# Kernel optimization log

Measured on AMD Instinct MI355X. Metric: run time of the kernel, lower is better.

Reference implementation:

```python
import jax, jax.numpy as jnp
import numpy as np

B, C, N, T = 8, 64, 170, 512
LEAK = 0.01
TEMP = 0.5


def _conv2d(x, w, b):
    # x: [B,C,N,Tp], w: [O,I,1,k] -> valid conv along time
    y = jax.lax.conv_general_dilated(x, w, (1, 1), 'VALID',
                                     dimension_numbers=('NCHW', 'OIHW', 'NCHW'))
    return y + b[None, :, None, None]


def _branch(x, w5, b5, w3, b3):
    # ReplicationPad2d((3,3,0,0)) -> Conv(1,5) -> LeakyReLU -> Conv(1,3) -> Tanh
    xp = jnp.pad(x, ((0, 0), (0, 0), (0, 0), (3, 3)), mode='edge')
    h = _conv2d(xp, w5, b5)
    h = jnp.where(h >= 0, h, LEAK * h)
    h = _conv2d(h, w3, b3)
    return jnp.tanh(h)


def _diff_gcn(x, adj, w, b):
    # Diffusion_GCN, support_len=1, order=1: concat([x, x@adj]) -> 1x1 conv
    x1 = jnp.einsum('bcnt,nm->bcmt', x, adj)
    h = jnp.concatenate([x, x1], axis=1)  # [B,2C,N,T]
    return jnp.einsum('bknt,ok->bont', h, w[:, :, 0, 0]) + b[None, :, None, None]


def _gumbel(k, shape, eps=1e-20):
    u = jax.random.uniform(k, shape, jnp.float32)
    return -jnp.log(-jnp.log(u + eps) + eps)


def _graph_gen(x, adj, g, ggw, ggb, fc0w, fc0b, fc1w, fc1b, fc2w, fc2b):
    h = _diff_gcn(x, adj, ggw, ggb)          # [B,C,N,T]
    h = h[-1].sum(-1).T                      # last batch elem, sum over T -> [N,C]
    h = jnp.tanh(h @ fc0w.T + fc0b)
    h = jnp.tanh(h @ fc1w.T + fc1b)
    h = jnp.tanh(h @ fc2w.T + fc2b)
    logp = jax.nn.log_softmax(h, axis=-1)
    y_soft = jax.nn.softmax((logp + g) / TEMP, axis=-1)
    y_hard = jax.nn.one_hot(jnp.argmax(y_soft, axis=-1), y_soft.shape[-1], dtype=y_soft.dtype)
    y = jax.lax.stop_gradient(y_hard - y_soft) + y_soft  # straight-through
    return y * (1.0 - jnp.eye(y.shape[0], dtype=y.dtype))  # zero diagonal


def _forward(x, nv1, nv2, a, c1w5, c1b5, c1w3, c1b3, c2w5, c2b5, c2w3, c2b3,
             c3w5, c3b5, c3w3, c3b3, c4w5, c4b5, c4w3, c4b3,
             ggw, ggb, fc0w, fc0b, fc1w, fc1b, fc2w, fc2b, dcw, dcb, gs):
    adj = jax.nn.softmax(jax.nn.relu(nv1 @ nv2), axis=1)
    xe, xo = x[..., ::2], x[..., 1::2]
    gg = (ggw, ggb, fc0w, fc0b, fc1w, fc1b, fc2w, fc2b)

    def step(xin, w5, b5, w3, b3, g):
        h = _branch(xin, w5, b5, w3, b3)
        la = _graph_gen(h, adj, g, *gg)
        dadj = la * a + adj * (1.0 - a)
        return h + _diff_gcn(h, dadj, dcw, dcb), dadj

    x1, dadj = step(xe, c1w5, c1b5, c1w3, c1b3, gs[0])
    d = xo * jnp.tanh(x1)
    x2, dadj = step(xo, c2w5, c2b5, c2w3, c2b3, gs[1])
    c = xe * jnp.tanh(x2)
    x3, dadj = step(c, c3w5, c3b5, c3w3, c3b3, gs[2])
    x_odd_update = d - x3
    x4, dadj = step(d, c4w5, c4b5, c4w3, c4b3, gs[3])
    x_even_update = c + x4
    return x_even_update, x_odd_update, dadj


def setup_inputs() -> dict:
    key = jax.random.key(0)
    ks = jax.random.split(key, 16)

    def rn(i, shape, s):
        return jax.random.normal(ks[i], shape, jnp.float32) * s

    inp = {'x': rn(0, (B, C, N, T), 1.0),
           'nv1': rn(1, (N, 10), 1.0),
           'nv2': rn(2, (10, N), 1.0),
           'a': jnp.array([0.5], jnp.float32)}
    i = 3
    for p in ('c1', 'c2', 'c3', 'c4'):
        inp[p + 'w5'] = rn(i, (C, C, 1, 5), 0.05); i += 1
        inp[p + 'b5'] = jnp.zeros((C,), jnp.float32)
        inp[p + 'w3'] = rn(i, (C, C, 1, 3), 0.05); i += 1
        inp[p + 'b3'] = jnp.zeros((C,), jnp.float32)
    inp['ggw'] = rn(i, (C, 2 * C, 1, 1), 0.08); i += 1
    inp['ggb'] = jnp.zeros((C,), jnp.float32)
    inp['fc0w'] = rn(i, (N, C), 0.1); i += 1
    inp['fc0b'] = jnp.zeros((N,), jnp.float32)
    inp['fc1w'] = rn(i, (2 * N, N), 0.06); i += 1
    inp['fc1b'] = jnp.zeros((2 * N,), jnp.float32)
    inp['fc2w'] = rn(i, (N, 2 * N), 0.05); i += 1
    inp['fc2b'] = jnp.zeros((N,), jnp.float32)
    inp['dcw'] = rn(i, (C, 2 * C, 1, 1), 0.08); i += 1
    inp['dcb'] = jnp.zeros((C,), jnp.float32)
    return inp


def reference(x, nv1, nv2, a, c1w5, c1b5, c1w3, c1b3, c2w5, c2b5, c2w3, c2b3,
              c3w5, c3b5, c3w3, c3b3, c4w5, c4b5, c4w3, c4b3,
              ggw, ggb, fc0w, fc0b, fc1w, fc1b, fc2w, fc2b, dcw, dcb):
    n = nv1.shape[0]
    gk = jax.random.split(jax.random.key(42), 4)
    gs = tuple(_gumbel(k, (n, n)) for k in gk)
    return _forward(x, nv1, nv2, a, c1w5, c1b5, c1w3, c1b3, c2w5, c2b5, c2w3, c2b3,
                    c3w5, c3b5, c3w3, c3b3, c4w5, c4b5, c4w3, c4b3,
                    ggw, ggb, fc0w, fc0b, fc1w, fc1b, fc2w, fc2b, dcw, dcb, gs)
```

## Files before the change

### kernel.cpp

```cpp
#include <hip/hip_runtime.h>
#include <hip/hip_bf16.h>
#include <cstdint>
#include <cstddef>

using bf16 = __hip_bfloat16;

static constexpr int BBATCH = 8, CCH = 64, NNODE = 170, TT = 256;
static constexpr size_t HSZ  = (size_t)BBATCH * CCH * NNODE * TT;
static constexpr size_t H7SZ = (size_t)CCH * NNODE * TT;
static constexpr int GN = NNODE * NNODE;

typedef __attribute__((ext_vector_type(8))) short short8v;
typedef __attribute__((ext_vector_type(4))) float f32x4;

__device__ __forceinline__ float b2f(bf16 v) { return __bfloat162float(v); }
__device__ __forceinline__ bf16  f2b(float v) { return __float2bfloat16(v); }

union BfU { bf16 h; unsigned short s; };
__device__ __forceinline__ unsigned short bfbits(float v) { BfU u; u.h = f2b(v); return u.s; }
__device__ __forceinline__ unsigned pack2(float a, float b) {
  return ((unsigned)bfbits(b) << 16) | bfbits(a);
}
__device__ __forceinline__ unsigned pks(short lo, short hi) {
  return ((unsigned)(unsigned short)hi << 16) | (unsigned short)lo;
}
__device__ __forceinline__ float shortbf(short s) { BfU u; u.s = (unsigned short)s; return b2f(u.h); }

__device__ __forceinline__ float tanhfast(float v) {
  float e = __expf(2.f * v);
  return 1.f - 2.f / (e + 1.f);
}

__device__ __forceinline__ unsigned rotl32(unsigned v, int d) { return (v << d) | (v >> (32 - d)); }

__device__ void threefry2x32(unsigned k0, unsigned k1, unsigned x0, unsigned x1,
                             unsigned& y0, unsigned& y1) {
  unsigned ks0 = k0, ks1 = k1, ks2 = k0 ^ k1 ^ 0x1BD11BDAu;
  x0 += ks0; x1 += ks1;
  const int ra[4] = {13, 15, 26, 6};
  const int rb[4] = {17, 29, 16, 24};
#pragma unroll
  for (int r = 0; r < 4; r++) { x0 += x1; x1 = rotl32(x1, ra[r]); x1 ^= x0; }
  x0 += ks1; x1 += ks2 + 1u;
#pragma unroll
  for (int r = 0; r < 4; r++) { x0 += x1; x1 = rotl32(x1, rb[r]); x1 ^= x0; }
  x0 += ks2; x1 += ks0 + 2u;
#pragma unroll
  for (int r = 0; r < 4; r++) { x0 += x1; x1 = rotl32(x1, ra[r]); x1 ^= x0; }
  x0 += ks0; x1 += ks1 + 3u;
#pragma unroll
  for (int r = 0; r < 4; r++) { x0 += x1; x1 = rotl32(x1, rb[r]); x1 ^= x0; }
  x0 += ks1; x1 += ks2 + 4u;
#pragma unroll
  for (int r = 0; r < 4; r++) { x0 += x1; x1 = rotl32(x1, ra[r]); x1 ^= x0; }
  x0 += ks2; x1 += ks0 + 5u;
  y0 = x0; y1 = x1;
}

struct SetupArgs {
  const float* w5[4]; const float* w3[4];
  float* wT5[4]; float* wT3[4];
  short* wp5[4]; short* wp3[4];
  const float* dcw; short* dcwP;
  const float* nv1; const float* nv2; float* adj;
  float* g;
};

__global__ __launch_bounds__(256) void k_setup(SetupArgs a) {
  const int blk = blockIdx.x;
  const int tid = threadIdx.x;
  __shared__ float red[256];

  if (blk < 170) {
    const int i = blk, j = tid;
    float val = 0.f, r = -1e30f;
    if (j < NNODE) {
      float acc = 0.f;
      for (int k = 0; k < 10; k++) acc += a.nv1[i*10+k] * a.nv2[k*NNODE+j];
      val = acc > 0.f ? acc : 0.f;
      r = val;
    }
    red[j] = r; __syncthreads();
    for (int s = 128; s; s >>= 1) { if (j < s) red[j] = fmaxf(red[j], red[j+s]); __syncthreads(); }
    float m = red[0]; __syncthreads();
    float e = (j < NNODE) ? expf(val - m) : 0.f;
    red[j] = e; __syncthreads();
    for (int s = 128; s; s >>= 1) { if (j < s) red[j] += red[j+s]; __syncthreads(); }
    if (j < NNODE) a.adj[i*NNODE+j] = e / red[0];
    return;
  }
  if (blk < 622) {
    int idx = (blk - 170) * 256 + tid;
    if (idx >= 4 * GN) return;
    int w = idx / GN, i = idx % GN;
    unsigned k0, k1, y0, y1;
    threefry2x32(0u, 42u, 0u, (unsigned)w, k0, k1);
    threefry2x32(k0, k1, 0u, (unsigned)i, y0, y1);
    unsigned bits = y0 ^ y1;
    unsigned fb = (bits >> 9) | 0x3f800000u;
    float u = __uint_as_float(fb) - 1.0f;
    a.g[idx] = -logf(-logf(u + 1e-20f) + 1e-20f);
    return;
  }
  if (blk < 942) {
    int gi = blk - 622, s = gi / 80;
    int idx = (gi - s*80) * 256 + tid;
    if (idx >= 20480) return;
    int oc = idx / 5, k = idx - oc * 5;
    int o = oc >> 6, c = oc & 63;
    a.wT5[s][(c*5 + k)*64 + o] = a.w5[s][idx];
    return;
  }
  if (blk < 1134) {
    int gi = blk - 942, s = gi / 48;
    int idx = (gi - s*48) * 256 + tid;
    if (idx >= 12288) return;
    int oc = idx / 3, k = idx - oc * 3;
    int o = oc >> 6, c = oc & 63;
    a.wT3[s][(c*3 + k)*64 + o] = a.w3[s][idx];
    return;
  }
  if (blk < 1454) {
    int gi = blk - 1134, s = gi / 80;
    int idx = (gi - s*80) * 256 + tid;
    if (idx >= 20480) return;
    int j = idx & 7, l = (idx >> 3) & 63, mi = (idx >> 9) & 3, ks = (idx >> 11) & 1, k = idx >> 12;
    int o = mi*16 + (l & 15);
    int c = ks*32 + (l >> 4)*8 + j;
    a.wp5[s][idx] = (short)bfbits(a.w5[s][(o*64 + c)*5 + k]);
    return;
  }
  if (blk < 1646) {
    int gi = blk - 1454, s = gi / 48;
    int idx = (gi - s*48) * 256 + tid;
    if (idx >= 12288) return;
    int j = idx & 7, l = (idx >> 3) & 63, mi = (idx >> 9) & 3, ks = (idx >> 11) & 1, k = idx >> 12;
    int o = mi*16 + (l & 15);
    int c = ks*32 + (l >> 4)*8 + j;
    a.wp3[s][idx] = (short)bfbits(a.w3[s][(o*64 + c)*3 + k]);
    return;
  }
  {
    int idx = (blk - 1646) * 256 + tid;
    if (idx >= 8192) return;
    int j = idx & 7, l = (idx >> 3) & 63, mi = (idx >> 9) & 3, kk = idx >> 11;
    int o = mi*16 + (l & 15);
    int c = kk*32 + (l >> 4)*8 + j;
    a.dcwP[idx] = (short)bfbits(a.dcw[o*128 + c]);
  }
}

__device__ void branch_body(int n, int q, int b,
    const float* __restrict__ src, int par,
    const float* __restrict__ wT5, const float* __restrict__ b5,
    const float* __restrict__ wT3, const float* __restrict__ b3,
    const short* __restrict__ wp5, const short* __restrict__ wp3,
    bf16* __restrict__ hout, float* __restrict__ h7f, float* __restrict__ Spart,
    char* lds) {
  const int tid = threadIdx.x;
  const int l = tid & 63;
  const int w = __builtin_amdgcn_readfirstlane(tid >> 6);
  const int t0 = q * 64;

  if (b == 7) {
    float (*xs)[72]  = (float(*)[72])lds;
    float (*h1s)[68] = (float(*)[68])(lds + 18432);
    const int o = l;
    const int base = w * 16;
    const bool w3x = (w == 3);

    for (int i = tid; i < 64 * 70; i += 256) {
      int c = i / 70, pl = i - c * 70;
      int t = t0 + pl - 3; t = t < 0 ? 0 : (t > 255 ? 255 : t);
      size_t sb = ((size_t)7 * 64 + c) * NNODE + n;
      xs[c][pl] = (par >= 0) ? src[sb * 512 + 2 * t + par] : src[sb * 256 + t];
    }
    __syncthreads();

    {
      float acc[16];
#pragma unroll
      for (int tt = 0; tt < 16; tt++) acc[tt] = 0.f;
      float aH0 = 0.f, aH1 = 0.f;
      const float* wp = wT5 + o;
      for (int c = 0; c < 64; c++) {
        float xv[22];
        float4 v0 = *(const float4*)&xs[c][base + 0];
        float4 v1 = *(const float4*)&xs[c][base + 4];
        float4 v2 = *(const float4*)&xs[c][base + 8];
        float4 v3 = *(const float4*)&xs[c][base + 12];
        float4 v4 = *(const float4*)&xs[c][base + 16];
        xv[0]=v0.x; xv[1]=v0.y; xv[2]=v0.z; xv[3]=v0.w;
        xv[4]=v1.x; xv[5]=v1.y; xv[6]=v1.z; xv[7]=v1.w;
        xv[8]=v2.x; xv[9]=v2.y; xv[10]=v2.z; xv[11]=v2.w;
        xv[12]=v3.x; xv[13]=v3.y; xv[14]=v3.z; xv[15]=v3.w;
        xv[16]=v4.x; xv[17]=v4.y; xv[18]=v4.z; xv[19]=v4.w;
        if (w3x) { float2 vt = *(const float2*)&xs[c][68]; xv[20]=vt.x; xv[21]=vt.y; }
        float w0 = wp[0], w1 = wp[64], w2 = wp[128], w3_ = wp[192], w4 = wp[256];
        wp += 320;
#pragma unroll
        for (int tt = 0; tt < 16; tt++)
          acc[tt] += w0*xv[tt] + w1*xv[tt+1] + w2*xv[tt+2] + w3_*xv[tt+3] + w4*xv[tt+4];
        if (w3x) {
          aH0 += w0*xv[16] + w1*xv[17] + w2*xv[18] + w3_*xv[19] + w4*xv[20];
          aH1 += w0*xv[17] + w1*xv[18] + w2*xv[19] + w3_*xv[20] + w4*xv[21];
        }
      }
      float bias = b5[o];
#pragma unroll
      for (int tt = 0; tt < 16; tt++) {
        float v = acc[tt] + bias;
        h1s[o][base + tt] = v >= 0.f ? v : 0.01f * v;
      }
      if (w3x) {
        float u0 = aH0 + bias, u1 = aH1 + bias;
        h1s[o][64] = u0 >= 0.f ? u0 : 0.01f * u0;
        h1s[o][65] = u1 >= 0.f ? u1 : 0.01f * u1;
      }
    }
    __syncthreads();

    {
      float acc[16];
#pragma unroll
      for (int tt = 0; tt < 16; tt++) acc[tt] = 0.f;
      const float* wp = wT3 + o;
      for (int c = 0; c < 64; c++) {
        float hv[18];
        float4 v0 = *(const float4*)&h1s[c][base + 0];
        float4 v1 = *(const float4*)&h1s[c][base + 4];
        float4 v2 = *(const float4*)&h1s[c][base + 8];
        float4 v3 = *(const float4*)&h1s[c][base + 12];
        float4 v4 = *(const float4*)&h1s[c][base + 16];
        hv[0]=v0.x; hv[1]=v0.y; hv[2]=v0.z; hv[3]=v0.w;
        hv[4]=v1.x; hv[5]=v1.y; hv[6]=v1.z; hv[7]=v1.w;
        hv[8]=v2.x; hv[9]=v2.y; hv[10]=v2.z; hv[11]=v2.w;
        hv[12]=v3.x; hv[13]=v3.y; hv[14]=v3.z; hv[15]=v3.w;
        hv[16]=v4.x; hv[17]=v4.y;
        float w0 = wp[0], w1 = wp[64], w2 = wp[128];
        wp += 192;
#pragma unroll
        for (int tt = 0; tt < 16; tt++)
          acc[tt] += w0*hv[tt] + w1*hv[tt+1] + w2*hv[tt+2];
      }
      float bias = b3[o];
#pragma unroll
      for (int tt = 0; tt < 16; tt++) acc[tt] = tanhf(acc[tt] + bias);
      __syncthreads();
#pragma unroll
      for (int tt = 0; tt < 16; tt++) xs[o][base + tt] = acc[tt];
    }
    __syncthreads();

    {
      const int ro = tid >> 2, rq = tid & 3;
      float4 v0 = *(const float4*)&xs[ro][rq*16 + 0];
      float4 v1 = *(const float4*)&xs[ro][rq*16 + 4];
      float4 v2 = *(const float4*)&xs[ro][rq*16 + 8];
      float4 v3 = *(const float4*)&xs[ro][rq*16 + 12];
      float* dst = h7f + ((size_t)ro * NNODE + n) * TT + t0 + rq*16;
      *(float4*)&dst[0] = v0; *(float4*)&dst[4] = v1;
      *(float4*)&dst[8] = v2; *(float4*)&dst[12] = v3;
      float s = v0.x+v0.y+v0.z+v0.w + v1.x+v1.y+v1.z+v1.w
              + v2.x+v2.y+v2.z+v2.w + v3.x+v3.y+v3.z+v3.w;
      s += __shfl_xor(s, 1, 4);
      s += __shfl_xor(s, 2, 4);
      if (rq == 0) Spart[(q * 64 + ro) * NNODE + n] = s;
    }
    return;
  }

  const int mi = w;

  {
    int t = t0 + l - 3; t = t < 0 ? 0 : (t > 255 ? 255 : t);
#pragma unroll
    for (int it = 0; it < 8; it++) {
      int c0 = it * 8 + mi * 2;
      size_t sb = ((size_t)b * 64 + c0) * NNODE + n;
      float v0, v1;
      if (par >= 0) { v0 = src[sb * 512 + 2*t + par]; v1 = src[(sb + NNODE) * 512 + 2*t + par]; }
      else          { v0 = src[sb * 256 + t];         v1 = src[(sb + NNODE) * 256 + t]; }
      *(unsigned*)(lds + l*128 + ((2*c0) ^ ((l & 7) << 4))) = pack2(v0, v1);
    }
  }
  if (tid < 192) {
    int tr = 64 + (tid >> 5);
    int c0 = (tid & 31) * 2;
    int t = t0 + tr - 3; if (t > 255) t = 255;
    size_t sb = ((size_t)b * 64 + c0) * NNODE + n;
    float v0, v1;
    if (par >= 0) { v0 = src[sb * 512 + 2*t + par]; v1 = src[(sb + NNODE) * 512 + 2*t + par]; }
    else          { v0 = src[sb * 256 + t];         v1 = src[(sb + NNODE) * 256 + t]; }
    *(unsigned*)(lds + tr*128 + ((2*c0) ^ ((tr & 7) << 4))) = pack2(v0, v1);
  }
  __syncthreads();

  f32x4 acc[5];
#pragma unroll
  for (int i = 0; i < 5; i++) acc[i] = (f32x4){0.f, 0.f, 0.f, 0.f};
  for (int k = 0; k < 5; k++) {
#pragma unroll
    for (int ks = 0; ks < 2; ks++) {
      short8v af = *(const short8v*)(wp5 + (size_t)((((k*2 + ks)*4 + mi)*64 + l) * 8));
      const int c0 = ks*32 + (l >> 4)*8;
#pragma unroll
      for (int ni = 0; ni < 5; ni++) {
        int tr = ni*16 + (l & 15) + k;
        short8v bf = *(const short8v*)(lds + tr*128 + ((2*c0) ^ ((tr & 7) << 4)));
        acc[ni] = __builtin_amdgcn_mfma_f32_16x16x32_bf16(af, bf, acc[ni], 0, 0, 0);
      }
    }
  }
  {
    const int o0 = mi*16 + ((l >> 4) << 2);
    float4 bv = *(const float4*)&b5[o0];
    float bb[4] = {bv.x, bv.y, bv.z, bv.w};
#pragma unroll
    for (int ni = 0; ni < 4; ni++) {
      int tr = ni*16 + (l & 15);
      float v[4];
#pragma unroll
      for (int r = 0; r < 4; r++) {
        float u = acc[ni][r] + bb[r];
        v[r] = u >= 0.f ? u : 0.01f * u;
      }
      int colb = (2*o0) ^ ((tr & 7) << 4);
      *(uint2*)(lds + 10752 + tr*128 + colb) = make_uint2(pack2(v[0], v[1]), pack2(v[2], v[3]));
    }
    if ((l & 15) < 2) {
      int tr = 64 + (l & 15);
      float v[4];
#pragma unroll
      for (int r = 0; r < 4; r++) {
        float u = acc[4][r] + bb[r];
        v[r] = u >= 0.f ? u : 0.01f * u;
      }
      int colb = (2*o0) ^ ((tr & 7) << 4);
      *(uint2*)(lds + 10752 + tr*128 + colb) = make_uint2(pack2(v[0], v[1]), pack2(v[2], v[3]));
    }
  }
  __syncthreads();

  f32x4 acc3[4];
#pragma unroll
  for (int i = 0; i < 4; i++) acc3[i] = (f32x4){0.f, 0.f, 0.f, 0.f};
  for (int k = 0; k < 3; k++) {
#pragma unroll
    for (int ks = 0; ks < 2; ks++) {
      short8v af = *(const short8v*)(wp3 + (size_t)((((k*2 + ks)*4 + mi)*64 + l) * 8));
      const int c0 = ks*32 + (l >> 4)*8;
#pragma unroll
      for (int ni = 0; ni < 4; ni++) {
        int tr = ni*16 + (l & 15) + k;
        short8v bf = *(const short8v*)(lds + 10752 + tr*128 + ((2*c0) ^ ((tr & 7) << 4)));
        acc3[ni] = __builtin_amdgcn_mfma_f32_16x16x32_bf16(af, bf, acc3[ni], 0, 0, 0);
      }
    }
  }
  {
    const int o0 = mi*16 + ((l >> 4) << 2);
    float4 bv = *(const float4*)&b3[o0];
    float bb[4] = {bv.x, bv.y, bv.z, bv.w};
#pragma unroll
    for (int ni = 0; ni < 4; ni++) {
      int t = ni*16 + (l & 15);
#pragma unroll
      for (int r = 0; r < 4; r++) {
        float v = tanhfast(acc3[ni][r] + bb[r]);
        *(short*)(lds + (o0 + r)*144 + t*2) = (short)bfbits(v);
      }
    }
  }
  __syncthreads();

  {
    const int ro = tid >> 2, rq = tid & 3;
    uint4 p0 = *(const uint4*)(lds + ro*144 + rq*32);
    uint4 p1 = *(const uint4*)(lds + ro*144 + rq*32 + 16);
    bf16* dst = hout + (((size_t)b * 64 + ro) * NNODE + n) * TT + t0 + rq*16;
    *(uint4*)&dst[0] = p0;
    *(uint4*)&dst[8] = p1;
  }
}

__global__ __launch_bounds__(256) void k_branch2(
    const float* src0, const float* src1, int par0, int par1,
    const float* wT5_0, const float* wT5_1, const float* b5_0, const float* b5_1,
    const float* wT3_0, const float* wT3_1, const float* b3_0, const float* b3_1,
    const short* wp5_0, const short* wp5_1, const short* wp3_0, const short* wp3_1,
    bf16* hout0, bf16* hout1, float* h7f0, float* h7f1, float* Sp0, float* Sp1) {
  __shared__ char lds[35840];
  int step, b;
  if (blockIdx.z < 2) { step = blockIdx.z; b = 7; }
  else { int zz = blockIdx.z - 2; step = zz / 7; b = zz % 7; }
  branch_body(blockIdx.x, blockIdx.y, b,
              step ? src1 : src0, step ? par1 : par0,
              step ? wT5_1 : wT5_0, step ? b5_1 : b5_0,
              step ? wT3_1 : wT3_0, step ? b3_1 : b3_0,
              step ? wp5_1 : wp5_0, step ? wp3_1 : wp3_0,
              step ? hout1 : hout0, step ? h7f1 : h7f0, step ? Sp1 : Sp0, lds);
}

__global__ __launch_bounds__(256) void k_sredT2(const float* __restrict__ Sp0, const float* __restrict__ Sp1,
                                                float* __restrict__ ST0, float* __restrict__ ST1) {
  int gidx = blockIdx.x * 256 + threadIdx.x;
  int step = gidx >= CCH*NNODE;
  int idx = gidx - step * CCH*NNODE;
  if (idx >= CCH * NNODE) return;
  const float* Sp = step ? Sp1 : Sp0;
  float* ST = step ? ST1 : ST0;
  int nn = idx >> 6, c = idx & 63;
  float acc = 0.f;
#pragma unroll
  for (int qq = 0; qq < 4; qq++) acc += Sp[(qq * 64 + c) * NNODE + nn];
  ST[idx] = acc;
}

__global__ __launch_bounds__(256) void k_gg2(const float* __restrict__ ST0, const float* __restrict__ ST1,
    const float* __restrict__ adj,
    const float* __restrict__ ggw, const float* __restrict__ ggb,
    const float* __restrict__ fc0w, const float* __restrict__ fc0b,
    const float* __restrict__ fc1w, const float* __restrict__ fc1b,
    const float* __restrict__ fc2w, const float* __restrict__ fc2b,
    const float* __restrict__ g0, const float* __restrict__ g1,
    const float* __restrict__ a_in,
    float* __restrict__ dadj0, float* __restrict__ dadj1,
    float* __restrict__ tail0, float* __restrict__ tail1) {
  const int i = blockIdx.x;
  const int step = blockIdx.y;
  const float* ST = step ? ST1 : ST0;
  const float* g = step ? g1 : g0;
  float* dadj = step ? dadj1 : dadj0;
  float* out_tail = step ? tail1 : tail0;
  const int tid = threadIdx.x;
  __shared__ float s1[64], sc[64], h0r[64];
  __shared__ float a1r[NNODE];
  __shared__ float a2r[340];
  __shared__ float vred[256];
  __shared__ int ired[256];
  if (tid < 64) {
    const int c = tid;
    float acc = 0.f;
    for (int nn = 0; nn < NNODE; nn++) acc += ST[nn*64 + c] * adj[nn*NNODE + i];
    s1[c] = acc;
    sc[c] = ST[i*64 + c];
  }
  __syncthreads();
  if (tid < 64) {
    const int o = tid;
    float acc = 256.f * ggb[o];
    for (int c = 0; c < 64; c++)
      acc += ggw[o*128 + c] * sc[c] + ggw[o*128 + 64 + c] * s1[c];
    h0r[o] = acc;
  }
  __syncthreads();
  if (tid < NNODE) {
    float acc = fc0b[tid];
    for (int o = 0; o < 64; o++) acc += h0r[o] * fc0w[tid*64 + o];
    a1r[tid] = tanhf(acc);
  }
  __syncthreads();
  for (int j = tid; j < 340; j += 256) {
    float acc = fc1b[j];
    for (int k = 0; k < NNODE; k++) acc += a1r[k] * fc1w[j*NNODE + k];
    a2r[j] = tanhf(acc);
  }
  __syncthreads();
  float v = -1e30f;
  if (tid < NNODE) {
    float acc = fc2b[tid];
    for (int k = 0; k < 340; k++) acc += a2r[k] * fc2w[tid*340 + k];
    v = tanhf(acc) + g[i*NNODE + tid];
  }
  vred[tid] = v; ired[tid] = tid;
  __syncthreads();
  for (int s = 128; s; s >>= 1) {
    if (tid < s) {
      if (vred[tid+s] > vred[tid]) { vred[tid] = vred[tid+s]; ired[tid] = ired[tid+s]; }
    }
    __syncthreads();
  }
  int jmax = ired[0];
  float a = a_in[0];
  if (tid < NNODE) {
    float la = (tid == jmax && jmax != i) ? 1.f : 0.f;
    float dv = la * a + adj[i*NNODE + tid] * (1.f - a);
    dadj[i*NNODE + tid] = dv;
    if (out_tail) out_tail[i*NNODE + tid] = dv;
  }
}

__global__ __launch_bounds__(256) void k_packD2(const float* __restrict__ dadj0, const float* __restrict__ dadj1,
                                                short* __restrict__ out0, short* __restrict__ out1) {
  int gidx = blockIdx.x * 256 + threadIdx.x;
  int step = gidx >= 33792;
  int idx = gidx - step * 33792;
  if (idx >= 33792) return;
  const float* dadj = step ? dadj1 : dadj0;
  short* out = step ? out1 : out0;
  int j = idx & 7, l = (idx >> 3) & 63;
  int g = idx >> 9;
  int ks = g % 6, mi = g / 6;
  int m = mi*16 + (l & 15);
  int n = ks*32 + (l >> 4)*8 + j;
  float v = (m < NNODE && n < NNODE) ? dadj[n*NNODE + m] : 0.f;
  out[idx] = (short)bfbits(v);
}

__global__ __launch_bounds__(256) void k_hA_m2(const bf16* __restrict__ h0, const short* __restrict__ dP0, bf16* __restrict__ hA0,
                                               const bf16* __restrict__ h1, const short* __restrict__ dP1, bf16* __restrict__ hA1) {
  const int step = blockIdx.z;
  const bf16* h = step ? h1 : h0;
  const short* dP = step ? dP1 : dP0;
  bf16* hA = step ? hA1 : hA0;
  const int bc = blockIdx.x, tq = blockIdx.y;
  const int tid = threadIdx.x;
  const int l = tid & 63;
  const int w = __builtin_amdgcn_readfirstlane(tid >> 6);
  const int t0 = tq * 64;
  __shared__ char lds[25600];

  const bf16* hp = h + (size_t)bc * NNODE * TT;
  for (int i = tid; i < 170*64; i += 256) {
    int n = i >> 6, t = i & 63;
    *(short*)(lds + t*400 + ((2*n) ^ ((t & 7) << 4))) = *(const short*)&hp[(size_t)n * TT + t0 + t];
  }
  for (int i = tid; i < 22*64; i += 256) {
    int n = 170 + (i >> 6), t = i & 63;
    *(short*)(lds + t*400 + ((2*n) ^ ((t & 7) << 4))) = 0;
  }
  __syncthreads();

  f32x4 acc[11];
#pragma unroll
  for (int i = 0; i < 11; i++) acc[i] = (f32x4){0.f, 0.f, 0.f, 0.f};
  const int tr = w*16 + (l & 15);
#pragma unroll
  for (int ks = 0; ks < 6; ks++) {
    const int n0 = ks*32 + (l >> 4)*8;
    short8v bf = *(const short8v*)(lds + tr*400 + ((2*n0) ^ ((tr & 7) << 4)));
#pragma unroll
    for (int mi = 0; mi < 11; mi++) {
      short8v af = *(const short8v*)(dP + (size_t)(((mi*6 + ks)*64 + l) * 8));
      acc[mi] = __builtin_amdgcn_mfma_f32_16x16x32_bf16(af, bf, acc[mi], 0, 0, 0);
    }
  }

  bf16* dst = hA + (size_t)bc * NNODE * TT + t0 + w*16 + (l & 15);
#pragma unroll
  for (int mi = 0; mi < 11; mi++) {
#pragma unroll
    for (int r = 0; r < 4; r++) {
      int m = mi*16 + ((l >> 4) << 2) + r;
      if (m < NNODE) dst[(size_t)m * TT] = f2b(acc[mi][r]);
    }
  }
}

__global__ __launch_bounds__(256) void k_hA7_2(const float* __restrict__ h7f0, const float* __restrict__ dadj0, float* __restrict__ hA7f0,
                                               const float* __restrict__ h7f1, const float* __restrict__ dadj1, float* __restrict__ hA7f1) {
  const int step = blockIdx.z;
  const float* h7f = step ? h7f1 : h7f0;
  const float* dadj = step ? dadj1 : dadj0;
  float* hA7f = step ? hA7f1 : hA7f0;
  const int c = blockIdx.x, tq = blockIdx.y;
  const int t0 = tq * 32;
  const int tid = threadIdx.x;
  const int lane = tid & 63;
  const int w = __builtin_amdgcn_readfirstlane(tid >> 6);
  __shared__ float hs[170][33];
  for (int i = tid; i < 170*32; i += 256) {
    int nn = i >> 5, tl = i & 31;
    hs[nn][tl] = h7f[((size_t)c * NNODE + nn) * TT + t0 + tl];
  }
  __syncthreads();
  float acc0[8], acc1[8], acc2[8];
#pragma unroll
  for (int tt = 0; tt < 8; tt++) { acc0[tt] = 0.f; acc1[tt] = 0.f; acc2[tt] = 0.f; }
  const int toff = w * 8;
  for (int nn = 0; nn < NNODE; nn++) {
    float hv[8];
#pragma unroll
    for (int tt = 0; tt < 8; tt++) hv[tt] = hs[nn][toff + tt];
    const float* dr = &dadj[nn * NNODE];
    float w0 = dr[lane];
    float w1 = dr[64 + lane];
    float w2 = (lane < 42) ? dr[128 + lane] : 0.f;
#pragma unroll
    for (int tt = 0; tt < 8; tt++) {
      acc0[tt] += w0 * hv[tt];
      acc1[tt] += w1 * hv[tt];
      acc2[tt] += w2 * hv[tt];
    }
  }
  __syncthreads();
#pragma unroll
  for (int tt = 0; tt < 8; tt++) {
    hs[lane][toff + tt] = acc0[tt];
    hs[64 + lane][toff + tt] = acc1[tt];
    if (lane < 42) hs[128 + lane][toff + tt] = acc2[tt];
  }
  __syncthreads();
  if (tid < NNODE) {
    float* dst = hA7f + ((size_t)c * NNODE + tid) * TT + t0;
#pragma unroll
    for (int j = 0; j < 8; j++)
      *(float4*)&dst[j*4] = make_float4(hs[tid][j*4], hs[tid][j*4+1], hs[tid][j*4+2], hs[tid][j*4+3]);
  }
}

__global__ __launch_bounds__(256) void k_mix_m2(const bf16* __restrict__ h0, const bf16* __restrict__ hA0,
                                                const bf16* __restrict__ h1, const bf16* __restrict__ hA1,
                                                const short* __restrict__ dcwP, const float* __restrict__ dcb,
                                                const float* __restrict__ x,
                                                float* __restrict__ oute, float* __restrict__ outo, int epiBase) {
  const int n = blockIdx.x, tq = blockIdx.z;
  const int b = blockIdx.y % 7;
  const int step = blockIdx.y / 7;
  const bf16* h = step ? h1 : h0;
  const bf16* hA = step ? hA1 : hA0;
  const int epi = epiBase + step;
  const int tid = threadIdx.x;
  const int l = tid & 63;
  const int mi = __builtin_amdgcn_readfirstlane(tid >> 6);
  const int t0 = tq * 64;
  __shared__ char lds[16384];

#pragma unroll
  for (int it = 0; it < 8; it++) {
    int c0 = it * 8 + mi * 2;
    size_t off = (((size_t)b * 64 + c0) * NNODE + n) * TT + t0 + l;
    size_t off1 = off + (size_t)NNODE * TT;
    *(unsigned*)(lds + l*256 + ((2*c0) ^ ((l & 7) << 4))) =
        pks(*(const short*)&h[off], *(const short*)&h[off1]);
    *(unsigned*)(lds + l*256 + ((2*(64 + c0)) ^ ((l & 7) << 4))) =
        pks(*(const short*)&hA[off], *(const short*)&hA[off1]);
  }
  __syncthreads();

  f32x4 acc[4];
#pragma unroll
  for (int i = 0; i < 4; i++) acc[i] = (f32x4){0.f, 0.f, 0.f, 0.f};
#pragma unroll
  for (int kk = 0; kk < 4; kk++) {
    short8v af = *(const short8v*)(dcwP + (size_t)(((kk*4 + mi)*64 + l) * 8));
    const int c0 = kk*32 + (l >> 4)*8;
#pragma unroll
    for (int ni = 0; ni < 4; ni++) {
      int tr = ni*16 + (l & 15);
      short8v bf = *(const short8v*)(lds + tr*256 + ((2*c0) ^ ((tr & 7) << 4)));
      acc[ni] = __builtin_amdgcn_mfma_f32_16x16x32_bf16(af, bf, acc[ni], 0, 0, 0);
    }
  }

  const int o0 = mi*16 + ((l >> 4) << 2);
  float dcb4[4];
#pragma unroll
  for (int r = 0; r < 4; r++) dcb4[r] = dcb[o0 + r];
#pragma unroll
  for (int ni = 0; ni < 4; ni++) {
    int t = ni*16 + (l & 15);
#pragma unroll
    for (int r = 0; r < 4; r++) {
      const int o = o0 + r;
      float hres = shortbf(*(const short*)(lds + t*256 + ((2*o) ^ ((t & 7) << 4))));
      float v = acc[ni][r] + hres + dcb4[r];
      size_t oidx = (((size_t)b * 64 + o) * NNODE + n) * TT + t0 + t;
      if (epi == 1) {
        outo[oidx] = x[(((size_t)b * 64 + o) * NNODE + n) * 512 + 2*(t0 + t) + 1] * tanhfast(v);
      } else if (epi == 2) {
        oute[oidx] = x[(((size_t)b * 64 + o) * NNODE + n) * 512 + 2*(t0 + t)] * tanhfast(v);
      } else if (epi == 3) {
        outo[oidx] -= v;
      } else {
        oute[oidx] += v;
      }
    }
  }
}

__global__ __launch_bounds__(256) void k_mix7_2(const float* __restrict__ h7f0, const float* __restrict__ hA7f0,
                                                const float* __restrict__ h7f1, const float* __restrict__ hA7f1,
                                                const float* __restrict__ dcw, const float* __restrict__ dcb,
                                                const float* __restrict__ x,
                                                float* __restrict__ oute, float* __restrict__ outo, int epiBase) {
  const int n = blockIdx.x;
  const int tq = blockIdx.y & 3;
  const int step = blockIdx.y >> 2;
  const float* h7f = step ? h7f1 : h7f0;
  const float* hA7f = step ? hA7f1 : hA7f0;
  const int epi = epiBase + step;
  const int tid = threadIdx.x;
  const int lane = tid & 63;
  const int w = __builtin_amdgcn_readfirstlane(tid >> 6);
  const int t = tq * 64 + lane;
  __shared__ float wTs[128][64];
  __shared__ float hsf[64][64];
  __shared__ float hasf[64][64];
  for (int i = tid; i < 8192; i += 256) {
    int o_ = i & 63, cf_ = i >> 6;
    wTs[cf_][o_] = dcw[o_*128 + cf_];
  }
  for (int i = tid; i < 4096; i += 256) {
    int c = i >> 6, tl = i & 63;
    size_t off = ((size_t)c * NNODE + n) * TT + tq * 64 + tl;
    hsf[c][tl] = h7f[off];
    hasf[c][tl] = hA7f[off];
  }
  __syncthreads();
  const int o0 = w * 16;
  float acc[16];
#pragma unroll
  for (int oo = 0; oo < 16; oo++) acc[oo] = 0.f;
  for (int cc = 0; cc < 64; cc++) {
    float hv = hsf[cc][lane];
    float hav = hasf[cc][lane];
    float4 wh0 = *(const float4*)&wTs[cc][o0 + 0];
    float4 wh1 = *(const float4*)&wTs[cc][o0 + 4];
    float4 wh2 = *(const float4*)&wTs[cc][o0 + 8];
    float4 wh3 = *(const float4*)&wTs[cc][o0 + 12];
    float4 wa0 = *(const float4*)&wTs[64 + cc][o0 + 0];
    float4 wa1 = *(const float4*)&wTs[64 + cc][o0 + 4];
    float4 wa2 = *(const float4*)&wTs[64 + cc][o0 + 8];
    float4 wa3 = *(const float4*)&wTs[64 + cc][o0 + 12];
    acc[0]  += wh0.x*hv + wa0.x*hav;  acc[1]  += wh0.y*hv + wa0.y*hav;
    acc[2]  += wh0.z*hv + wa0.z*hav;  acc[3]  += wh0.w*hv + wa0.w*hav;
    acc[4]  += wh1.x*hv + wa1.x*hav;  acc[5]  += wh1.y*hv + wa1.y*hav;
    acc[6]  += wh1.z*hv + wa1.z*hav;  acc[7]  += wh1.w*hv + wa1.w*hav;
    acc[8]  += wh2.x*hv + wa2.x*hav;  acc[9]  += wh2.y*hv + wa2.y*hav;
    acc[10] += wh2.z*hv + wa2.z*hav;  acc[11] += wh2.w*hv + wa2.w*hav;
    acc[12] += wh3.x*hv + wa3.x*hav;  acc[13] += wh3.y*hv + wa3.y*hav;
    acc[14] += wh3.z*hv + wa3.z*hav;  acc[15] += wh3.w*hv + wa3.w*hav;
  }
#pragma unroll
  for (int oo = 0; oo < 16; oo++) {
    const int o = o0 + oo;
    float v = acc[oo] + hsf[o][lane] + dcb[o];
    size_t oidx = (((size_t)7 * 64 + o) * NNODE + n) * TT + t;
    if (epi == 1) {
      outo[oidx] = x[(((size_t)7 * 64 + o) * NNODE + n) * 512 + 2*t + 1] * tanhf(v);
    } else if (epi == 2) {
      oute[oidx] = x[(((size_t)7 * 64 + o) * NNODE + n) * 512 + 2*t] * tanhf(v);
    } else if (epi == 3) {
      outo[oidx] -= v;
    } else {
      oute[oidx] += v;
    }
  }
}

extern "C" void kernel_launch(void* const* d_in, const int* in_sizes, int n_in,
                              void* d_out, int out_size, void* d_ws, size_t ws_size,
                              hipStream_t stream) {
  const float* x    = (const float*)d_in[0];
  const float* nv1  = (const float*)d_in[1];
  const float* nv2  = (const float*)d_in[2];
  const float* a_in = (const float*)d_in[3];
  const float *w5[4], *b5[4], *w3[4], *b3[4];
  for (int s = 0; s < 4; s++) {
    w5[s] = (const float*)d_in[4 + 4*s];
    b5[s] = (const float*)d_in[5 + 4*s];
    w3[s] = (const float*)d_in[6 + 4*s];
    b3[s] = (const float*)d_in[7 + 4*s];
  }
  const float* ggw  = (const float*)d_in[20];
  const float* ggb  = (const float*)d_in[21];
  const float* fc0w = (const float*)d_in[22];
  const float* fc0b = (const float*)d_in[23];
  const float* fc1w = (const float*)d_in[24];
  const float* fc1b = (const float*)d_in[25];
  const float* fc2w = (const float*)d_in[26];
  const float* fc2b = (const float*)d_in[27];
  const float* dcw  = (const float*)d_in[28];
  const float* dcb  = (const float*)d_in[29];

  char* p = (char*)d_ws;
  size_t used = 0;
  auto alloc = [&](size_t bytes) -> char* {
    char* r = p + used;
    used += (bytes + 255) & ~(size_t)255;
    return r;
  };
  float* adjW   = (float*)alloc(GN*4);
  float* dadjA  = (float*)alloc(GN*4);
  float* dadjB  = (float*)alloc(GN*4);
  float* gW     = (float*)alloc(4*GN*4);
  float* STa    = (float*)alloc(CCH*NNODE*4);
  float* STb    = (float*)alloc(CCH*NNODE*4);
  float* SpA    = (float*)alloc(4*CCH*NNODE*4);
  float* SpB    = (float*)alloc(4*CCH*NNODE*4);
  float* wT5[4]; float* wT3[4];
  short* wp5[4]; short* wp3[4];
  for (int s = 0; s < 4; s++) {
    wT5[s] = (float*)alloc(64*64*5*4);
    wT3[s] = (float*)alloc(64*64*3*4);
    wp5[s] = (short*)alloc(20480*2);
    wp3[s] = (short*)alloc(12288*2);
  }
  short* dcwP   = (short*)alloc(8192*2);
  short* dPA    = (short*)alloc(33792*2);
  short* dPB    = (short*)alloc(33792*2);
  bf16* H1      = (bf16*)alloc(HSZ*2);
  bf16* H2      = (bf16*)alloc(HSZ*2);
  bf16* HAa     = (bf16*)alloc(HSZ*2);
  float* h7fA   = (float*)alloc(H7SZ*4);
  float* h7fB   = (float*)alloc(H7SZ*4);
  float* hA7fA  = (float*)alloc(H7SZ*4);
  if (used > ws_size) return;

  bf16* HAb; float* hA7fB; bool merged;
  {
    size_t need = used + ((HSZ*2 + 255) & ~(size_t)255) + ((H7SZ*4 + 255) & ~(size_t)255);
    if (need <= ws_size) {
      HAb   = (bf16*)alloc(HSZ*2);
      hA7fB = (float*)alloc(H7SZ*4);
      merged = true;
    } else {
      HAb = HAa; hA7fB = hA7fA; merged = false;
    }
  }

  float* oute = (float*)d_out;
  float* outo = oute + HSZ;
  float* tail = oute + 2*HSZ;

  SetupArgs sa;
  for (int s = 0; s < 4; s++) {
    sa.w5[s] = w5[s]; sa.w3[s] = w3[s];
    sa.wT5[s] = wT5[s]; sa.wT3[s] = wT3[s];
    sa.wp5[s] = wp5[s]; sa.wp3[s] = wp3[s];
  }
  sa.dcw = dcw; sa.dcwP = dcwP;
  sa.nv1 = nv1; sa.nv2 = nv2; sa.adj = adjW;
  sa.g = gW;
  k_setup<<<1678, 256, 0, stream>>>(sa);

  dim3 bgrid2(NNODE, 4, 16);

  auto phase = [&](const float* srcA, const float* srcB, int parA, int parB,
                   int sA, int sB, const float* gA, const float* gB,
                   float* tailB, int epiBase) {
    k_branch2<<<bgrid2, 256, 0, stream>>>(srcA, srcB, parA, parB,
        wT5[sA], wT5[sB], b5[sA], b5[sB], wT3[sA], wT3[sB], b3[sA], b3[sB],
        wp5[sA], wp5[sB], wp3[sA], wp3[sB],
        H1, H2, h7fA, h7fB, SpA, SpB);
    k_sredT2<<<86, 256, 0, stream>>>(SpA, SpB, STa, STb);
    k_gg2<<<dim3(NNODE, 2), 256, 0, stream>>>(STa, STb, adjW, ggw, ggb,
        fc0w, fc0b, fc1w, fc1b, fc2w, fc2b, gA, gB, a_in,
        dadjA, dadjB, nullptr, tailB);
    k_packD2<<<264, 256, 0, stream>>>(dadjA, dadjB, dPA, dPB);
    if (merged) {
      k_hA_m2<<<dim3(448, 4, 2), 256, 0, stream>>>(H1, dPA, HAa, H2, dPB, HAb);
      k_hA7_2<<<dim3(64, 8, 2), 256, 0, stream>>>(h7fA, dadjA, hA7fA, h7fB, dadjB, hA7fB);
      k_mix_m2<<<dim3(NNODE, 14, 4), 256, 0, stream>>>(H1, HAa, H2, HAb, dcwP, dcb, x, oute, outo, epiBase);
      k_mix7_2<<<dim3(NNODE, 8), 256, 0, stream>>>(h7fA, hA7fA, h7fB, hA7fB, dcw, dcb, x, oute, outo, epiBase);
    } else {
      k_hA_m2<<<dim3(448, 4, 1), 256, 0, stream>>>(H1, dPA, HAa, H1, dPA, HAa);
      k_hA7_2<<<dim3(64, 8, 1), 256, 0, stream>>>(h7fA, dadjA, hA7fA, h7fA, dadjA, hA7fA);
      k_mix_m2<<<dim3(NNODE, 7, 4), 256, 0, stream>>>(H1, HAa, H1, HAa, dcwP, dcb, x, oute, outo, epiBase);
      k_mix7_2<<<dim3(NNODE, 4), 256, 0, stream>>>(h7fA, hA7fA, h7fA, hA7fA, dcw, dcb, x, oute, outo, epiBase);
      k_hA_m2<<<dim3(448, 4, 1), 256, 0, stream>>>(H2, dPB, HAa, H2, dPB, HAa);
      k_hA7_2<<<dim3(64, 8, 1), 256, 0, stream>>>(h7fB, dadjB, hA7fA, h7fB, dadjB, hA7fA);
      k_mix_m2<<<dim3(NNODE, 7, 4), 256, 0, stream>>>(H2, HAa, H2, HAa, dcwP, dcb, x, oute, outo, epiBase + 1);
      k_mix7_2<<<dim3(NNODE, 4), 256, 0, stream>>>(h7fB, hA7fA, h7fB, hA7fA, dcw, dcb, x, oute, outo, epiBase + 1);
    }
  };

  phase(x, x, 0, 1, 0, 1, gW, gW + GN, nullptr, 1);

  phase(oute, outo, -1, -1, 2, 3, gW + 2*GN, gW + 3*GN, tail, 3);

  (void)in_sizes; (void)n_in; (void)out_size;
}
```

Before: 1.234 ms.

## Split batch-7 branch into finer time tiles and fuse adjacency packing into graph kernel

The fp32 batch-7 branch path now runs in 32-step time tiles, which doubles its block count and shrinks the shared-memory footprint. That path is separated from the MFMA branch body, and the LDS allocation is reduced so more blocks can be resident at once. The packed bf16 copy of dadj is now written directly inside k_gg2, which removes the separate k_packD2 launch; the packed buffers are zeroed once in setup so their padding stays valid. In exchange, the partial-sum buffers double in size, there is an extra barrier in branchM, and the packed stores from k_gg2 are scattered.

```diff
diff --git a/kernel.cpp b/kernel.cpp
--- a/kernel.cpp
+++ b/kernel.cpp
@@ -64,6 +64,7 @@
   const float* dcw; short* dcwP;
   const float* nv1; const float* nv2; float* adj;
   float* g;
+  short* dPA; short* dPB;
 };
 
 __global__ __launch_bounds__(256) void k_setup(SetupArgs a) {
@@ -140,137 +141,137 @@
     a.wp3[s][idx] = (short)bfbits(a.w3[s][(o*64 + c)*3 + k]);
     return;
   }
-  {
+  if (blk < 1678) {
     int idx = (blk - 1646) * 256 + tid;
     if (idx >= 8192) return;
     int j = idx & 7, l = (idx >> 3) & 63, mi = (idx >> 9) & 3, kk = idx >> 11;
     int o = mi*16 + (l & 15);
     int c = kk*32 + (l >> 4)*8 + j;
     a.dcwP[idx] = (short)bfbits(a.dcw[o*128 + c]);
-  }
-}
-
-__device__ void branch_body(int n, int q, int b,
+    return;
+  }
+  {
+    int idx = (blk - 1678) * 256 + tid;
+    if (idx < 33792) a.dPA[idx] = 0;
+    else if (idx < 67584) a.dPB[idx - 33792] = 0;
+  }
+}
+
+__device__ void branch7_body(int n, int q,
     const float* __restrict__ src, int par,
     const float* __restrict__ wT5, const float* __restrict__ b5,
     const float* __restrict__ wT3, const float* __restrict__ b3,
-    const short* __restrict__ wp5, const short* __restrict__ wp3,
-    bf16* __restrict__ hout, float* __restrict__ h7f, float* __restrict__ Spart,
-    char* lds) {
+    float* __restrict__ h7f, float* __restrict__ Spart, char* lds) {
   const int tid = threadIdx.x;
   const int l = tid & 63;
   const int w = __builtin_amdgcn_readfirstlane(tid >> 6);
+  const int t0 = q * 32;
+  float (*xs)[40]  = (float(*)[40])lds;
+  float (*h1s)[36] = (float(*)[36])(lds + 10240);
+  const int o = l;
+  const int base = w * 8;
+  const bool w3x = (w == 3);
+
+  for (int i = tid; i < 64 * 38; i += 256) {
+    int c = i / 38, pl = i - c * 38;
+    int t = t0 + pl - 3; t = t < 0 ? 0 : (t > 255 ? 255 : t);
+    size_t sb = ((size_t)7 * 64 + c) * NNODE + n;
+    xs[c][pl] = (par >= 0) ? src[sb * 512 + 2 * t + par] : src[sb * 256 + t];
+  }
+  __syncthreads();
+
+  {
+    float acc[8];
+#pragma unroll
+    for (int tt = 0; tt < 8; tt++) acc[tt] = 0.f;
+    float aH0 = 0.f, aH1 = 0.f;
+    const float* wp = wT5 + o;
+    for (int c = 0; c < 64; c++) {
+      float xv[14];
+      float4 v0 = *(const float4*)&xs[c][base + 0];
+      float4 v1 = *(const float4*)&xs[c][base + 4];
+      float4 v2 = *(const float4*)&xs[c][base + 8];
+      xv[0]=v0.x; xv[1]=v0.y; xv[2]=v0.z; xv[3]=v0.w;
+      xv[4]=v1.x; xv[5]=v1.y; xv[6]=v1.z; xv[7]=v1.w;
+      xv[8]=v2.x; xv[9]=v2.y; xv[10]=v2.z; xv[11]=v2.w;
+      if (w3x) { float2 vt = *(const float2*)&xs[c][36]; xv[12]=vt.x; xv[13]=vt.y; }
+      float w0 = wp[0], w1 = wp[64], w2 = wp[128], w3_ = wp[192], w4 = wp[256];
+      wp += 320;
+#pragma unroll
+      for (int tt = 0; tt < 8; tt++)
+        acc[tt] += w0*xv[tt] + w1*xv[tt+1] + w2*xv[tt+2] + w3_*xv[tt+3] + w4*xv[tt+4];
+      if (w3x) {
+        aH0 += w0*xv[8] + w1*xv[9] + w2*xv[10] + w3_*xv[11] + w4*xv[12];
+        aH1 += w0*xv[9] + w1*xv[10] + w2*xv[11] + w3_*xv[12] + w4*xv[13];
+      }
+    }
+    float bias = b5[o];
+#pragma unroll
+    for (int tt = 0; tt < 8; tt++) {
+      float v = acc[tt] + bias;
+      h1s[o][base + tt] = v >= 0.f ? v : 0.01f * v;
+    }
+    if (w3x) {
+      float u0 = aH0 + bias, u1 = aH1 + bias;
+      h1s[o][32] = u0 >= 0.f ? u0 : 0.01f * u0;
+      h1s[o][33] = u1 >= 0.f ? u1 : 0.01f * u1;
+    }
+  }
+  __syncthreads();
+
+  {
+    float acc[8];
+#pragma unroll
+    for (int tt = 0; tt < 8; tt++) acc[tt] = 0.f;
+    const float* wp = wT3 + o;
+    for (int c = 0; c < 64; c++) {
+      float hv[10];
+      float4 v0 = *(const float4*)&h1s[c][base + 0];
+      float4 v1 = *(const float4*)&h1s[c][base + 4];
+      float2 v2 = *(const float2*)&h1s[c][base + 8];
+      hv[0]=v0.x; hv[1]=v0.y; hv[2]=v0.z; hv[3]=v0.w;
+      hv[4]=v1.x; hv[5]=v1.y; hv[6]=v1.z; hv[7]=v1.w;
+      hv[8]=v2.x; hv[9]=v2.y;
+      float w0 = wp[0], w1 = wp[64], w2 = wp[128];
+      wp += 192;
+#pragma unroll
+      for (int tt = 0; tt < 8; tt++)
+        acc[tt] += w0*hv[tt] + w1*hv[tt+1] + w2*hv[tt+2];
+    }
+    float bias = b3[o];
+#pragma unroll
+    for (int tt = 0; tt < 8; tt++) acc[tt] = tanhf(acc[tt] + bias);
+    __syncthreads();
+#pragma unroll
+    for (int tt = 0; tt < 8; tt++) xs[o][base + tt] = acc[tt];
+  }
+  __syncthreads();
+
+  if (tid < 128) {
+    const int ro = tid >> 1, rq = tid & 1;
+    float4 v0 = *(const float4*)&xs[ro][rq*16 + 0];
+    float4 v1 = *(const float4*)&xs[ro][rq*16 + 4];
+    float4 v2 = *(const float4*)&xs[ro][rq*16 + 8];
+    float4 v3 = *(const float4*)&xs[ro][rq*16 + 12];
+    float* dst = h7f + ((size_t)ro * NNODE + n) * TT + t0 + rq*16;
+    *(float4*)&dst[0] = v0; *(float4*)&dst[4] = v1;
+    *(float4*)&dst[8] = v2; *(float4*)&dst[12] = v3;
+    float s = v0.x+v0.y+v0.z+v0.w + v1.x+v1.y+v1.z+v1.w
+            + v2.x+v2.y+v2.z+v2.w + v3.x+v3.y+v3.z+v3.w;
+    s += __shfl_xor(s, 1, 2);
+    if (rq == 0) Spart[(q * 64 + ro) * NNODE + n] = s;
+  }
+}
+
+__device__ void branchM_body(int n, int q, int b,
+    const float* __restrict__ src, int par,
+    const float* __restrict__ b5, const float* __restrict__ b3,
+    const short* __restrict__ wp5, const short* __restrict__ wp3,
+    bf16* __restrict__ hout, char* lds) {
+  const int tid = threadIdx.x;
+  const int l = tid & 63;
+  const int mi = __builtin_amdgcn_readfirstlane(tid >> 6);
   const int t0 = q * 64;
-
-  if (b == 7) {
-    float (*xs)[72]  = (float(*)[72])lds;
-    float (*h1s)[68] = (float(*)[68])(lds + 18432);
-    const int o = l;
-    const int base = w * 16;
-    const bool w3x = (w == 3);
-
-    for (int i = tid; i < 64 * 70; i += 256) {
-      int c = i / 70, pl = i - c * 70;
-      int t = t0 + pl - 3; t = t < 0 ? 0 : (t > 255 ? 255 : t);
-      size_t sb = ((size_t)7 * 64 + c) * NNODE + n;
-      xs[c][pl] = (par >= 0) ? src[sb * 512 + 2 * t + par] : src[sb * 256 + t];
-    }
-    __syncthreads();
-
-    {
-      float acc[16];
-#pragma unroll
-      for (int tt = 0; tt < 16; tt++) acc[tt] = 0.f;
-      float aH0 = 0.f, aH1 = 0.f;
-      const float* wp = wT5 + o;
-      for (int c = 0; c < 64; c++) {
-        float xv[22];
-        float4 v0 = *(const float4*)&xs[c][base + 0];
-        float4 v1 = *(const float4*)&xs[c][base + 4];
-        float4 v2 = *(const float4*)&xs[c][base + 8];
-        float4 v3 = *(const float4*)&xs[c][base + 12];
-        float4 v4 = *(const float4*)&xs[c][base + 16];
-        xv[0]=v0.x; xv[1]=v0.y; xv[2]=v0.z; xv[3]=v0.w;
-        xv[4]=v1.x; xv[5]=v1.y; xv[6]=v1.z; xv[7]=v1.w;
-        xv[8]=v2.x; xv[9]=v2.y; xv[10]=v2.z; xv[11]=v2.w;
-        xv[12]=v3.x; xv[13]=v3.y; xv[14]=v3.z; xv[15]=v3.w;
-        xv[16]=v4.x; xv[17]=v4.y; xv[18]=v4.z; xv[19]=v4.w;
-        if (w3x) { float2 vt = *(const float2*)&xs[c][68]; xv[20]=vt.x; xv[21]=vt.y; }
-        float w0 = wp[0], w1 = wp[64], w2 = wp[128], w3_ = wp[192], w4 = wp[256];
-        wp += 320;
-#pragma unroll
-        for (int tt = 0; tt < 16; tt++)
-          acc[tt] += w0*xv[tt] + w1*xv[tt+1] + w2*xv[tt+2] + w3_*xv[tt+3] + w4*xv[tt+4];
-        if (w3x) {
-          aH0 += w0*xv[16] + w1*xv[17] + w2*xv[18] + w3_*xv[19] + w4*xv[20];
-          aH1 += w0*xv[17] + w1*xv[18] + w2*xv[19] + w3_*xv[20] + w4*xv[21];
-        }
-      }
-      float bias = b5[o];
-#pragma unroll
-      for (int tt = 0; tt < 16; tt++) {
-        float v = acc[tt] + bias;
-        h1s[o][base + tt] = v >= 0.f ? v : 0.01f * v;
-      }
-      if (w3x) {
-        float u0 = aH0 + bias, u1 = aH1 + bias;
-        h1s[o][64] = u0 >= 0.f ? u0 : 0.01f * u0;
-        h1s[o][65] = u1 >= 0.f ? u1 : 0.01f * u1;
-      }
-    }
-    __syncthreads();
-
-    {
-      float acc[16];
-#pragma unroll
-      for (int tt = 0; tt < 16; tt++) acc[tt] = 0.f;
-      const float* wp = wT3 + o;
-      for (int c = 0; c < 64; c++) {
-        float hv[18];
-        float4 v0 = *(const float4*)&h1s[c][base + 0];
-        float4 v1 = *(const float4*)&h1s[c][base + 4];
-        float4 v2 = *(const float4*)&h1s[c][base + 8];
-        float4 v3 = *(const float4*)&h1s[c][base + 12];
-        float4 v4 = *(const float4*)&h1s[c][base + 16];
-        hv[0]=v0.x; hv[1]=v0.y; hv[2]=v0.z; hv[3]=v0.w;
-        hv[4]=v1.x; hv[5]=v1.y; hv[6]=v1.z; hv[7]=v1.w;
-        hv[8]=v2.x; hv[9]=v2.y; hv[10]=v2.z; hv[11]=v2.w;
-        hv[12]=v3.x; hv[13]=v3.y; hv[14]=v3.z; hv[15]=v3.w;
-        hv[16]=v4.x; hv[17]=v4.y;
-        float w0 = wp[0], w1 = wp[64], w2 = wp[128];
-        wp += 192;
-#pragma unroll
-        for (int tt = 0; tt < 16; tt++)
-          acc[tt] += w0*hv[tt] + w1*hv[tt+1] + w2*hv[tt+2];
-      }
-      float bias = b3[o];
-#pragma unroll
-      for (int tt = 0; tt < 16; tt++) acc[tt] = tanhf(acc[tt] + bias);
-      __syncthreads();
-#pragma unroll
-      for (int tt = 0; tt < 16; tt++) xs[o][base + tt] = acc[tt];
-    }
-    __syncthreads();
-
-    {
-      const int ro = tid >> 2, rq = tid & 3;
-      float4 v0 = *(const float4*)&xs[ro][rq*16 + 0];
-      float4 v1 = *(const float4*)&xs[ro][rq*16 + 4];
-      float4 v2 = *(const float4*)&xs[ro][rq*16 + 8];
-      float4 v3 = *(const float4*)&xs[ro][rq*16 + 12];
-      float* dst = h7f + ((size_t)ro * NNODE + n) * TT + t0 + rq*16;
-      *(float4*)&dst[0] = v0; *(float4*)&dst[4] = v1;
-      *(float4*)&dst[8] = v2; *(float4*)&dst[12] = v3;
-      float s = v0.x+v0.y+v0.z+v0.w + v1.x+v1.y+v1.z+v1.w
-              + v2.x+v2.y+v2.z+v2.w + v3.x+v3.y+v3.z+v3.w;
-      s += __shfl_xor(s, 1, 4);
-      s += __shfl_xor(s, 2, 4);
-      if (rq == 0) Spart[(q * 64 + ro) * NNODE + n] = s;
-    }
-    return;
-  }
-
-  const int mi = w;
 
   {
     int t = t0 + l - 3; t = t < 0 ? 0 : (t > 255 ? 255 : t);
@@ -362,6 +363,7 @@
     const int o0 = mi*16 + ((l >> 4) << 2);
     float4 bv = *(const float4*)&b3[o0];
     float bb[4] = {bv.x, bv.y, bv.z, bv.w};
+    __syncthreads();
 #pragma unroll
     for (int ni = 0; ni < 4; ni++) {
       int t = ni*16 + (l & 15);
@@ -390,16 +392,25 @@
     const float* wT3_0, const float* wT3_1, const float* b3_0, const float* b3_1,
     const short* wp5_0, const short* wp5_1, const short* wp3_0, const short* wp3_1,
     bf16* hout0, bf16* hout1, float* h7f0, float* h7f1, float* Sp0, float* Sp1) {
-  __shared__ char lds[35840];
-  int step, b;
-  if (blockIdx.z < 2) { step = blockIdx.z; b = 7; }
-  else { int zz = blockIdx.z - 2; step = zz / 7; b = zz % 7; }
-  branch_body(blockIdx.x, blockIdx.y, b,
-              step ? src1 : src0, step ? par1 : par0,
-              step ? wT5_1 : wT5_0, step ? b5_1 : b5_0,
-              step ? wT3_1 : wT3_0, step ? b3_1 : b3_0,
-              step ? wp5_1 : wp5_0, step ? wp3_1 : wp3_0,
-              step ? hout1 : hout0, step ? h7f1 : h7f0, step ? Sp1 : Sp0, lds);
+  __shared__ char lds[19456];
+  const int y = blockIdx.y;
+  if (y < 16) {
+    const int step = y >> 3, q = y & 7;
+    branch7_body(blockIdx.x, q,
+                 step ? src1 : src0, step ? par1 : par0,
+                 step ? wT5_1 : wT5_0, step ? b5_1 : b5_0,
+                 step ? wT3_1 : wT3_0, step ? b3_1 : b3_0,
+                 step ? h7f1 : h7f0, step ? Sp1 : Sp0, lds);
+  } else {
+    const int yy = y - 16;
+    const int step = yy / 28, rr = yy % 28;
+    const int b = rr >> 2, q = rr & 3;
+    branchM_body(blockIdx.x, q, b,
+                 step ? src1 : src0, step ? par1 : par0,
+                 step ? b5_1 : b5_0, step ? b3_1 : b3_0,
+                 step ? wp5_1 : wp5_0, step ? wp3_1 : wp3_0,
+                 step ? hout1 : hout0, lds);
+  }
 }
 
 __global__ __launch_bounds__(256) void k_sredT2(const float* __restrict__ Sp0, const float* __restrict__ Sp1,
@@ -413,7 +424,10 @@
   int nn = idx >> 6, c = idx & 63;
   float acc = 0.f;
 #pragma unroll
-  for (int qq = 0; qq < 4; qq++) acc += Sp[(qq * 64 + c) * NNODE + nn];
+  for (int qq = 0; qq < 4; qq++) {
+    float qv = Sp[((2*qq) * 64 + c) * NNODE + nn] + Sp[((2*qq + 1) * 64 + c) * NNODE + nn];
+    acc += qv;
+  }
   ST[idx] = acc;
 }
 
@@ -426,12 +440,14 @@
     const float* __restrict__ g0, const float* __restrict__ g1,
     const float* __restrict__ a_in,
     float* __restrict__ dadj0, float* __restrict__ dadj1,
+    short* __restrict__ dP0, short* __restrict__ dP1,
     float* __restrict__ tail0, float* __restrict__ tail1) {
   const int i = blockIdx.x;
   const int step = blockIdx.y;
   const float* ST = step ? ST1 : ST0;
   const float* g = step ? g1 : g0;
   float* dadj = step ? dadj1 : dadj0;
+  short* dP = step ? dP1 : dP0;
   float* out_tail = step ? tail1 : tail0;
   const int tid = threadIdx.x;
   __shared__ float s1[64], sc[64], h0r[64];
@@ -488,24 +504,11 @@
     float dv = la * a + adj[i*NNODE + tid] * (1.f - a);
     dadj[i*NNODE + tid] = dv;
     if (out_tail) out_tail[i*NNODE + tid] = dv;
-  }
-}
-
-__global__ __launch_bounds__(256) void k_packD2(const float* __restrict__ dadj0, const float* __restrict__ dadj1,
-                                                short* __restrict__ out0, short* __restrict__ out1) {
-  int gidx = blockIdx.x * 256 + threadIdx.x;
-  int step = gidx >= 33792;
-  int idx = gidx - step * 33792;
-  if (idx >= 33792) return;
-  const float* dadj = step ? dadj1 : dadj0;
-  short* out = step ? out1 : out0;
-  int j = idx & 7, l = (idx >> 3) & 63;
-  int g = idx >> 9;
-  int ks = g % 6, mi = g / 6;
-  int m = mi*16 + (l & 15);
-  int n = ks*32 + (l >> 4)*8 + j;
-  float v = (m < NNODE && n < NNODE) ? dadj[n*NNODE + m] : 0.f;
-  out[idx] = (short)bfbits(v);
+    const int ks = i >> 5, rem = i & 31;
+    const int lidx = ((rem >> 3) << 4) | (tid & 15);
+    const int mi = tid >> 4;
+    dP[(size_t)(((mi*6 + ks)*64 + lidx) * 8) + (rem & 7)] = (short)bfbits(dv);
+  }
 }
 
 __global__ __launch_bounds__(256) void k_hA_m2(const bf16* __restrict__ h0, const short* __restrict__ dP0, bf16* __restrict__ hA0,
@@ -788,8 +791,8 @@
   float* gW     = (float*)alloc(4*GN*4);
   float* STa    = (float*)alloc(CCH*NNODE*4);
   float* STb    = (float*)alloc(CCH*NNODE*4);
-  float* SpA    = (float*)alloc(4*CCH*NNODE*4);
-  float* SpB    = (float*)alloc(4*CCH*NNODE*4);
+  float* SpA    = (float*)alloc(8*CCH*NNODE*4);
+  float* SpB    = (float*)alloc(8*CCH*NNODE*4);
   float* wT5[4]; float* wT3[4];
   short* wp5[4]; short* wp3[4];
   for (int s = 0; s < 4; s++) {
@@ -834,9 +837,10 @@
   sa.dcw = dcw; sa.dcwP = dcwP;
   sa.nv1 = nv1; sa.nv2 = nv2; sa.adj = adjW;
   sa.g = gW;
-  k_setup<<<1678, 256, 0, stream>>>(sa);
-
-  dim3 bgrid2(NNODE, 4, 16);
+  sa.dPA = dPA; sa.dPB = dPB;
+  k_setup<<<1942, 256, 0, stream>>>(sa);
+
+  dim3 bgrid2(NNODE, 72);
 
   auto phase = [&](const float* srcA, const float* srcB, int parA, int parB,
                    int sA, int sB, const float* gA, const float* gB,
@@ -848,8 +852,7 @@
     k_sredT2<<<86, 256, 0, stream>>>(SpA, SpB, STa, STb);
     k_gg2<<<dim3(NNODE, 2), 256, 0, stream>>>(STa, STb, adjW, ggw, ggb,
         fc0w, fc0b, fc1w, fc1b, fc2w, fc2b, gA, gB, a_in,
-        dadjA, dadjB, nullptr, tailB);
-    k_packD2<<<264, 256, 0, stream>>>(dadjA, dadjB, dPA, dPB);
+        dadjA, dadjB, dPA, dPB, nullptr, tailB);
     if (merged) {
       k_hA_m2<<<dim3(448, 4, 2), 256, 0, stream>>>(H1, dPA, HAa, H2, dPB, HAb);
       k_hA7_2<<<dim3(64, 8, 2), 256, 0, stream>>>(h7fA, dadjA, hA7fA, h7fB, dadjB, hA7fB);
```

Result: slower. 1.307 ms (+5.9%).
